# Kernel tuning notes

Measured on AMD Instinct MI355X. Metric: run time of the kernel, lower is better.

## Reference

```python
import jax, jax.numpy as jnp
import numpy as np
from jax import lax

KERNEL = 15
IGNORE = 255


def setup_inputs() -> dict:
    key = jax.random.key(0)
    k1, k2 = jax.random.split(key)
    B, C, H, W = 32, 2, 480, 864
    logits = jax.random.normal(k1, (B, C, H, W), dtype=jnp.float32)
    labels = jax.random.randint(k2, (B, H, W), 0, 2, dtype=jnp.int32)
    return {"logits": logits, "labels": labels}


def _boundary_edgemap(labels):
    # labels: [B, H, W] int32 with values in {0, 1, IGNORE}
    lbl = labels.astype(jnp.int32)
    # np_label = label*255, with ignore pixels set to 0 (matches cv2 path)
    np_label = jnp.where(lbl == IGNORE, 0, lbl * 255)
    win = (1, KERNEL, KERNEL)
    strides = (1, 1, 1)
    # cv2.erode with ones kernel == 15x15 min filter (border value +inf -> pad 255)
    erosion = lax.reduce_window(np_label, jnp.int32(255), lax.min, win, strides, "SAME")
    # cv2.dilate == 15x15 max filter (border value -inf -> pad 0)
    dilation = lax.reduce_window(np_label, jnp.int32(0), lax.max, win, strides, "SAME")
    boundary = dilation - erosion  # >0 exactly on the morphological boundary band
    edgemap = jnp.where(boundary > 0, lbl, IGNORE)
    edgemap = jnp.where(lbl == IGNORE, IGNORE, edgemap)
    return edgemap


def reference(logits, labels):
    # logits: [B, C, H, W] log-probabilities, labels: [B, H, W]
    edgemap = _boundary_edgemap(labels)  # [B, H, W]
    valid = edgemap != IGNORE
    tgt = jnp.where(valid, edgemap, 0)  # safe index for ignored pixels
    # gather logits[b, tgt, h, w] -> [B, H, W]
    picked = jnp.take_along_axis(logits, tgt[:, None, :, :], axis=1)[:, 0]
    # NLLLoss with ignore_index: mean of -logp over valid pixels
    n_valid = jnp.maximum(jnp.sum(valid), 1)
    loss = -jnp.sum(jnp.where(valid, picked, 0.0)) / n_valid.astype(logits.dtype)
    return loss
```

## Files before the change

### kernel.cpp

```cpp
#include <hip/hip_runtime.h>


namespace {
constexpr int B_ = 32;
constexpr int H_ = 480;
constexpr int W_ = 864;
constexpr int HW = H_ * W_;
constexpr int R_ = 7;
constexpr int OC = 50;
constexpr int TH_ = 32;
constexpr int LH = TH_ + 2 * R_;
constexpr int NSX = (W_ + OC - 1) / OC;
constexpr int NSY = H_ / TH_;
constexpr int NTILE = B_ * NSY * NSX;
constexpr int WPB = 4;
constexpr int NBLKP = NTILE / WPB;
}

__device__ __forceinline__ unsigned hwin15(unsigned x) {
  unsigned a = x | __shfl_down(x, 1, 64);
  a |= __shfl_down(a, 2, 64);
  a |= __shfl_down(a, 4, 64);
  a |= __shfl_down(a, 7, 64);
  return __shfl_up(a, 7, 64);
}

extern "C" __global__ __launch_bounds__(256, 6)
void boundary_loss_main(const float* __restrict__ logits,
                        const int* __restrict__ labels,
                        double2* __restrict__ partials)
{
  __shared__ double red_s[WPB];
  __shared__ unsigned red_c[WPB];

  const int tid = threadIdx.x;
  const int lane = tid & 63;
  const int wv = tid >> 6;
  const int t = blockIdx.x * WPB + wv;
  const int b  = t / (NSY * NSX);
  const int rr = t - b * (NSY * NSX);
  const int sy = rr / NSX;
  const int sx = rr - sy * NSX;

  const int gr0 = sy * TH_;
  const int col = sx * OC - R_ + lane;
  const bool colok = (col >= 0) && (col < W_);
  const int colc = col < 0 ? 0 : (col >= W_ ? W_ - 1 : col);

  const int* __restrict__ lab = labels + b * HW;
  const float* __restrict__ lg = logits + (size_t)(2 * b) * HW;

  unsigned f0 = 0, f1 = 0, f2 = 0, c0 = 0, c1 = 0, c2 = 0;
#pragma unroll
  for (int a = 0; a < LH; ++a) {
    const int gr = gr0 - R_ + a;
    const int grc = gr < 0 ? 0 : (gr >= H_ ? H_ - 1 : gr);
    const int v = lab[grc * W_ + colc];
    unsigned f = (unsigned)((v == 0) | (v == 255)) | ((unsigned)(v == 1) << 1);
    const unsigned c = (unsigned)(v == 1) | ((unsigned)(v == 255) << 1);
    if (gr < 0 || gr >= H_) f = 0;
    const int sh = 2 * (a & 15);
    if (a < 16)      { f0 |= f << sh; c0 |= c << sh; }
    else if (a < 32) { f1 |= f << sh; c1 |= c << sh; }
    else             { f2 |= f << sh; c2 |= c << sh; }
  }
  if (!colok) { f0 = f1 = f2 = 0; }

  const unsigned h0 = hwin15(f0);
  const unsigned h1 = hwin15(f1);
  const unsigned h2 = hwin15(f2);

  unsigned long long A  = (unsigned long long)h0 | ((unsigned long long)h1 << 32);
  unsigned long long Bv = (unsigned long long)h1 | ((unsigned long long)h2 << 32);
  A  |= A  >> 2;  A  |= A  >> 4;  A  |= A  >> 8;  A  |= A  >> 14;
  Bv |= Bv >> 2;  Bv |= Bv >> 4;  Bv |= Bv >> 8;  Bv |= Bv >> 14;

  double lsum = 0.0;
  unsigned lcnt = 0;
  const bool outlane = (lane >= R_) && (lane < R_ + OC) && colok;
  if (outlane) {
    int lgoff = gr0 * W_ + colc;
#pragma unroll
    for (int o = 0; o < TH_; ++o, lgoff += W_) {
      const unsigned fb = (o < 18) ? ((unsigned)(A >> (2 * o)) & 3u)
                                   : ((unsigned)(Bv >> (2 * (o - 16))) & 3u);
      const int ar = o + R_;
      const unsigned creg = (ar < 16) ? c0 : (ar < 32 ? c1 : c2);
      const unsigned cb = (creg >> (2 * (ar & 15))) & 3u;
      const bool ok = (fb == 3u) && ((cb & 2u) == 0u);
      const float val = lg[lgoff + (int)(cb & 1u) * HW];
      lsum += ok ? (double)val : 0.0;
      lcnt += ok ? 1u : 0u;
    }
  }

#pragma unroll
  for (int off = 32; off > 0; off >>= 1) {
    lsum += __shfl_down(lsum, off, 64);
    lcnt += __shfl_down(lcnt, off, 64);
  }
  if ((tid & 63) == 0) { red_s[wv] = lsum; red_c[wv] = lcnt; }
  __syncthreads();
  if (tid == 0) {
    const double s = red_s[0] + red_s[1] + red_s[2] + red_s[3];
    const double c = (double)(red_c[0] + red_c[1] + red_c[2] + red_c[3]);
    partials[blockIdx.x] = make_double2(s, c);
  }
}

extern "C" __global__ __launch_bounds__(1024)
void boundary_loss_final(const double2* __restrict__ partials,
                         float* __restrict__ out)
{
  __shared__ double red_s[16];
  __shared__ double red_c[16];
  const int tid = threadIdx.x;
  double s = 0.0, c = 0.0;
  for (int i = tid; i < NBLKP; i += 1024) {
    const double2 p = partials[i];
    s += p.x;
    c += p.y;
  }
#pragma unroll
  for (int off = 32; off > 0; off >>= 1) {
    s += __shfl_down(s, off, 64);
    c += __shfl_down(c, off, 64);
  }
  const int wave = tid >> 6;
  if ((tid & 63) == 0) { red_s[wave] = s; red_c[wave] = c; }
  __syncthreads();
  if (tid == 0) {
    double ts = 0.0, tc = 0.0;
#pragma unroll
    for (int i = 0; i < 16; ++i) { ts += red_s[i]; tc += red_c[i]; }
    if (tc < 1.0) tc = 1.0;
    out[0] = (float)(-ts / tc);
  }
}

extern "C" void kernel_launch(void* const* d_in, const int* in_sizes, int n_in,
                              void* d_out, int out_size, void* d_ws, size_t ws_size,
                              hipStream_t stream)
{
  const float* logits = (const float*)d_in[0];
  const int* labels = (const int*)d_in[1];
  float* out = (float*)d_out;
  double2* partials = (double2*)d_ws;

  boundary_loss_main<<<dim3(NBLKP), 256, 0, stream>>>(logits, labels, partials);
  boundary_loss_final<<<1, 1024, 0, stream>>>(partials, out);
}
```

Before: 196.2 us.

## Vectorize tiles to 4 columns per lane with int4/float4 loads

Each lane now handles four adjacent columns, loading labels as int4 and both logit channels as float4. Tiles become 8 rows by 216 columns, so the horizontal 15-wide dilation is built from two-lane shuffles on 64-bit packed masks and vertical halo overhead changes. Both logit channels are loaded unconditionally instead of gathering the selected one, which removes per-pixel scalar gathers at the cost of more register pressure, doubled logit traffic, and a larger relative vertical halo (8 rows with 14 halo rows).

Result: slower. 221.0 us (+12.6%).

```diff
diff --git a/kernel.cpp b/kernel.cpp
--- a/kernel.cpp
+++ b/kernel.cpp
@@ -7,25 +7,24 @@
 constexpr int W_ = 864;
 constexpr int HW = H_ * W_;
 constexpr int R_ = 7;
-constexpr int OC = 50;
-constexpr int TH_ = 32;
+constexpr int TH_ = 8;
 constexpr int LH = TH_ + 2 * R_;
-constexpr int NSX = (W_ + OC - 1) / OC;
+constexpr int SW = 216;
+constexpr int NSX = W_ / SW;
 constexpr int NSY = H_ / TH_;
+constexpr int WPB = 4;
 constexpr int NTILE = B_ * NSY * NSX;
-constexpr int WPB = 4;
 constexpr int NBLKP = NTILE / WPB;
 }
 
-__device__ __forceinline__ unsigned hwin15(unsigned x) {
-  unsigned a = x | __shfl_down(x, 1, 64);
-  a |= __shfl_down(a, 2, 64);
-  a |= __shfl_down(a, 4, 64);
-  a |= __shfl_down(a, 7, 64);
-  return __shfl_up(a, 7, 64);
+__device__ __forceinline__ unsigned long long shfl_up64(unsigned long long x, int d) {
+  return __shfl_up(x, d, 64);
+}
+__device__ __forceinline__ unsigned long long shfl_dn64(unsigned long long x, int d) {
+  return __shfl_down(x, d, 64);
 }
 
-extern "C" __global__ __launch_bounds__(256, 6)
+extern "C" __global__ __launch_bounds__(256, 4)
 void boundary_loss_main(const float* __restrict__ logits,
                         const int* __restrict__ labels,
                         double2* __restrict__ partials)
@@ -37,60 +36,104 @@
   const int lane = tid & 63;
   const int wv = tid >> 6;
   const int t = blockIdx.x * WPB + wv;
-  const int b  = t / (NSY * NSX);
+  const int b = t / (NSY * NSX);
   const int rr = t - b * (NSY * NSX);
-  const int sy = rr / NSX;
-  const int sx = rr - sy * NSX;
+  const int sy = rr >> 2;
+  const int sx = rr & 3;
 
   const int gr0 = sy * TH_;
-  const int col = sx * OC - R_ + lane;
-  const bool colok = (col >= 0) && (col < W_);
-  const int colc = col < 0 ? 0 : (col >= W_ ? W_ - 1 : col);
+  const int wb = sx * SW - 8;
+  const int cb0 = wb + 4 * lane;
+  const bool colinb = (cb0 >= 0) && (cb0 + 3 < W_);
+  const int cbc = colinb ? cb0 : (cb0 < 0 ? 0 : W_ - 4);
 
-  const int* __restrict__ lab = labels + b * HW;
+  const int* __restrict__ lab = labels + b * HW + cbc;
   const float* __restrict__ lg = logits + (size_t)(2 * b) * HW;
 
-  unsigned f0 = 0, f1 = 0, f2 = 0, c0 = 0, c1 = 0, c2 = 0;
+  int4 lv[LH];
 #pragma unroll
   for (int a = 0; a < LH; ++a) {
-    const int gr = gr0 - R_ + a;
-    const int grc = gr < 0 ? 0 : (gr >= H_ ? H_ - 1 : gr);
-    const int v = lab[grc * W_ + colc];
-    unsigned f = (unsigned)((v == 0) | (v == 255)) | ((unsigned)(v == 1) << 1);
-    const unsigned c = (unsigned)(v == 1) | ((unsigned)(v == 255) << 1);
-    if (gr < 0 || gr >= H_) f = 0;
-    const int sh = 2 * (a & 15);
-    if (a < 16)      { f0 |= f << sh; c0 |= c << sh; }
-    else if (a < 32) { f1 |= f << sh; c1 |= c << sh; }
-    else             { f2 |= f << sh; c2 |= c << sh; }
+    int gr = gr0 - R_ + a;
+    gr = gr < 0 ? 0 : (gr >= H_ ? H_ - 1 : gr);
+    lv[a] = *(const int4*)(lab + gr * W_);
   }
-  if (!colok) { f0 = f1 = f2 = 0; }
 
-  const unsigned h0 = hwin15(f0);
-  const unsigned h1 = hwin15(f1);
-  const unsigned h2 = hwin15(f2);
+  unsigned long long f0 = 0, f1 = 0, f2 = 0, f3 = 0;
+  unsigned cp0 = 0, cp1 = 0, cp2 = 0, cp3 = 0;
+#pragma unroll
+  for (int a = 0; a < LH; ++a) {
+    const int4 v = lv[a];
+    const unsigned e1x = (v.x == 1), e1y = (v.y == 1),
+                   e1z = (v.z == 1), e1w = (v.w == 1);
+    f0 |= (unsigned long long)(1u + e1x) << (2 * a);
+    f1 |= (unsigned long long)(1u + e1y) << (2 * a);
+    f2 |= (unsigned long long)(1u + e1z) << (2 * a);
+    f3 |= (unsigned long long)(1u + e1w) << (2 * a);
+    if (a >= R_ && a < R_ + TH_) {
+      const int sh = 2 * (a - R_);
+      cp0 |= (e1x | ((unsigned)(v.x == 255) << 1)) << sh;
+      cp1 |= (e1y | ((unsigned)(v.y == 255) << 1)) << sh;
+      cp2 |= (e1z | ((unsigned)(v.z == 255) << 1)) << sh;
+      cp3 |= (e1w | ((unsigned)(v.w == 255) << 1)) << sh;
+    }
+  }
+  {
+    const int tv = gr0 == 0 ? R_ : 0;
+    const int hi = LH < (487 - gr0) ? LH : (487 - gr0);
+    unsigned long long rm = ((1ull << (2 * (hi - tv))) - 1ull) << (2 * tv);
+    if (!colinb) rm = 0;
+    f0 &= rm; f1 &= rm; f2 &= rm; f3 &= rm;
+  }
 
-  unsigned long long A  = (unsigned long long)h0 | ((unsigned long long)h1 << 32);
-  unsigned long long Bv = (unsigned long long)h1 | ((unsigned long long)h2 << 32);
-  A  |= A  >> 2;  A  |= A  >> 4;  A  |= A  >> 8;  A  |= A  >> 14;
-  Bv |= Bv >> 2;  Bv |= Bv >> 4;  Bv |= Bv >> 8;  Bv |= Bv >> 14;
+  const bool outl = (lane >= 2) && (lane < 56);
+  float4 g0[TH_], g1[TH_];
+  if (outl) {
+    const float* pg = lg + (size_t)gr0 * W_ + cb0;
+#pragma unroll
+    for (int o = 0; o < TH_; ++o) {
+      g0[o] = *(const float4*)(pg + o * W_);
+      g1[o] = *(const float4*)(pg + o * W_ + HW);
+    }
+  }
+
+  const unsigned long long allf = f0 | f1 | f2 | f3;
+  const unsigned long long s2 = f2 | f3, s3 = f1 | s2;
+  const unsigned long long p2 = f0 | f1, p3 = p2 | f2;
+  const unsigned long long core =
+      shfl_up64(allf, 1) | allf | shfl_dn64(allf, 1);
+  unsigned long long w0 = core | shfl_up64(s3, 2);
+  unsigned long long w1 = core | shfl_up64(s2, 2) | shfl_dn64(f0, 2);
+  unsigned long long w2 = core | shfl_up64(f3, 2) | shfl_dn64(p2, 2);
+  unsigned long long w3 = core | shfl_dn64(p3, 2);
+
+  w0 |= w0 >> 2;  w0 |= w0 >> 4;  w0 |= w0 >> 8;  w0 |= w0 >> 14;
+  w1 |= w1 >> 2;  w1 |= w1 >> 4;  w1 |= w1 >> 8;  w1 |= w1 >> 14;
+  w2 |= w2 >> 2;  w2 |= w2 >> 4;  w2 |= w2 >> 8;  w2 |= w2 >> 14;
+  w3 |= w3 >> 2;  w3 |= w3 >> 4;  w3 |= w3 >> 8;  w3 |= w3 >> 14;
 
   double lsum = 0.0;
   unsigned lcnt = 0;
-  const bool outlane = (lane >= R_) && (lane < R_ + OC) && colok;
-  if (outlane) {
-    int lgoff = gr0 * W_ + colc;
+  if (outl) {
 #pragma unroll
-    for (int o = 0; o < TH_; ++o, lgoff += W_) {
-      const unsigned fb = (o < 18) ? ((unsigned)(A >> (2 * o)) & 3u)
-                                   : ((unsigned)(Bv >> (2 * (o - 16))) & 3u);
-      const int ar = o + R_;
-      const unsigned creg = (ar < 16) ? c0 : (ar < 32 ? c1 : c2);
-      const unsigned cb = (creg >> (2 * (ar & 15))) & 3u;
-      const bool ok = (fb == 3u) && ((cb & 2u) == 0u);
-      const float val = lg[lgoff + (int)(cb & 1u) * HW];
-      lsum += ok ? (double)val : 0.0;
-      lcnt += ok ? 1u : 0u;
+    for (int o = 0; o < TH_; ++o) {
+      const unsigned b0 = (unsigned)(w0 >> (2 * o)) & 3u;
+      const unsigned b1 = (unsigned)(w1 >> (2 * o)) & 3u;
+      const unsigned b2 = (unsigned)(w2 >> (2 * o)) & 3u;
+      const unsigned b3 = (unsigned)(w3 >> (2 * o)) & 3u;
+      const unsigned q0 = (cp0 >> (2 * o)) & 3u;
+      const unsigned q1 = (cp1 >> (2 * o)) & 3u;
+      const unsigned q2 = (cp2 >> (2 * o)) & 3u;
+      const unsigned q3 = (cp3 >> (2 * o)) & 3u;
+      const float4 a = g0[o], c = g1[o];
+      const bool k0 = (b0 == 3u) && !(q0 & 2u);
+      const bool k1 = (b1 == 3u) && !(q1 & 2u);
+      const bool k2 = (b2 == 3u) && !(q2 & 2u);
+      const bool k3 = (b3 == 3u) && !(q3 & 2u);
+      lsum += k0 ? (double)((q0 & 1u) ? c.x : a.x) : 0.0;
+      lsum += k1 ? (double)((q1 & 1u) ? c.y : a.y) : 0.0;
+      lsum += k2 ? (double)((q2 & 1u) ? c.z : a.z) : 0.0;
+      lsum += k3 ? (double)((q3 & 1u) ? c.w : a.w) : 0.0;
+      lcnt += (unsigned)k0 + k1 + k2 + k3;
     }
   }
 
```

## Restructure boundary loss into 216-wide block tiles with vectorized loads and LDS bitplanes

Applied to the files above, without the earlier changes.

Each block now handles a 32x216 tile. Waves cooperatively load label rows as int4, packing four columns per lane into 2-bit flags, and build the horizontal window with neighbour shuffles. Per-column bitmasks go through a shared-memory plane so each wave can run the vertical window over its 8 output rows. Logits for both classes are prefetched unconditionally as float4 before the label work, and block IDs are swizzled across XCDs. This cuts redundant halo loads and scalar gathers, at the cost of reading both logit channels and a sync plus more LDS and registers per block.

Measured after the change: 199.9 us. No clear change (+1.9%).

```diff
diff --git a/kernel.cpp b/kernel.cpp
--- a/kernel.cpp
+++ b/kernel.cpp
@@ -7,90 +7,144 @@
 constexpr int W_ = 864;
 constexpr int HW = H_ * W_;
 constexpr int R_ = 7;
-constexpr int OC = 50;
 constexpr int TH_ = 32;
 constexpr int LH = TH_ + 2 * R_;
-constexpr int NSX = (W_ + OC - 1) / OC;
+constexpr int SW = 216;
+constexpr int NSX = W_ / SW;
 constexpr int NSY = H_ / TH_;
-constexpr int NTILE = B_ * NSY * NSX;
-constexpr int WPB = 4;
-constexpr int NBLKP = NTILE / WPB;
-}
-
-__device__ __forceinline__ unsigned hwin15(unsigned x) {
-  unsigned a = x | __shfl_down(x, 1, 64);
-  a |= __shfl_down(a, 2, 64);
-  a |= __shfl_down(a, 4, 64);
-  a |= __shfl_down(a, 7, 64);
-  return __shfl_up(a, 7, 64);
-}
-
-extern "C" __global__ __launch_bounds__(256, 6)
+constexpr int NBLK = B_ * NSY * NSX;
+constexpr int ROWP = 50;
+}
+
+typedef unsigned long long u64;
+
+extern "C" __global__ __launch_bounds__(256, 4)
 void boundary_loss_main(const float* __restrict__ logits,
                         const int* __restrict__ labels,
                         double2* __restrict__ partials)
 {
-  __shared__ double red_s[WPB];
-  __shared__ unsigned red_c[WPB];
+  __shared__ unsigned short plane[64][ROWP];
+  __shared__ double red_s[4];
+  __shared__ unsigned red_c[4];
 
   const int tid = threadIdx.x;
   const int lane = tid & 63;
   const int wv = tid >> 6;
-  const int t = blockIdx.x * WPB + wv;
-  const int b  = t / (NSY * NSX);
-  const int rr = t - b * (NSY * NSX);
-  const int sy = rr / NSX;
-  const int sx = rr - sy * NSX;
-
+  const int bid = blockIdx.x;
+  const int lb = (bid & 7) * (NBLK / 8) + (bid >> 3);
+  const int b = lb / (NSY * NSX);
+  const int rr = lb - b * (NSY * NSX);
+  const int sy = rr >> 2;
+  const int sx = rr & 3;
   const int gr0 = sy * TH_;
-  const int col = sx * OC - R_ + lane;
-  const bool colok = (col >= 0) && (col < W_);
-  const int colc = col < 0 ? 0 : (col >= W_ ? W_ - 1 : col);
+  const int colbase = sx * SW;
 
   const int* __restrict__ lab = labels + b * HW;
   const float* __restrict__ lg = logits + (size_t)(2 * b) * HW;
 
-  unsigned f0 = 0, f1 = 0, f2 = 0, c0 = 0, c1 = 0, c2 = 0;
-#pragma unroll
-  for (int a = 0; a < LH; ++a) {
-    const int gr = gr0 - R_ + a;
-    const int grc = gr < 0 ? 0 : (gr >= H_ ? H_ - 1 : gr);
-    const int v = lab[grc * W_ + colc];
-    unsigned f = (unsigned)((v == 0) | (v == 255)) | ((unsigned)(v == 1) << 1);
-    const unsigned c = (unsigned)(v == 1) | ((unsigned)(v == 255) << 1);
-    if (gr < 0 || gr >= H_) f = 0;
-    const int sh = 2 * (a & 15);
-    if (a < 16)      { f0 |= f << sh; c0 |= c << sh; }
-    else if (a < 32) { f1 |= f << sh; c1 |= c << sh; }
-    else             { f2 |= f << sh; c2 |= c << sh; }
-  }
-  if (!colok) { f0 = f1 = f2 = 0; }
-
-  const unsigned h0 = hwin15(f0);
-  const unsigned h1 = hwin15(f1);
-  const unsigned h2 = hwin15(f2);
-
-  unsigned long long A  = (unsigned long long)h0 | ((unsigned long long)h1 << 32);
-  unsigned long long Bv = (unsigned long long)h1 | ((unsigned long long)h2 << 32);
-  A  |= A  >> 2;  A  |= A  >> 4;  A  |= A  >> 8;  A  |= A  >> 14;
-  Bv |= Bv >> 2;  Bv |= Bv >> 4;  Bv |= Bv >> 8;  Bv |= Bv >> 14;
+  const bool outl = (lane >= 2) && (lane < 56);
+  float4 ga[8], gc[8];
+  {
+    const float* pg = lg + (size_t)(gr0 + 8 * wv) * W_ + (colbase + 4 * (lane - 2));
+    if (outl) {
+#pragma unroll
+      for (int o = 0; o < 8; ++o) {
+        ga[o] = *(const float4*)(pg + (size_t)o * W_);
+        gc[o] = *(const float4*)(pg + (size_t)o * W_ + HW);
+      }
+    }
+  }
+
+  const int r_lo = 12 * wv;
+  const int nr = (wv == 3) ? 10 : 12;
+  const int cb0 = colbase - 8 + 4 * lane;
+  const bool labok = (lane < 58) && (cb0 >= 0) && (cb0 + 3 < W_);
+  const int* labp = lab + (labok ? cb0 : 0);
+
+  unsigned f0 = 0, f1 = 0, f2 = 0, f3 = 0;
+  unsigned c0 = 0, c1 = 0, c2 = 0, c3 = 0;
+#pragma unroll
+  for (int k = 0; k < 12; ++k) {
+    if (k < nr) {
+      const int a = r_lo + k;
+      const int gr = gr0 - R_ + a;
+      const bool rowok = (gr >= 0) && (gr < H_);
+      const int grc = rowok ? gr : (gr < 0 ? 0 : H_ - 1);
+      const int4 v = *(const int4*)(labp + grc * W_);
+      const unsigned m = (labok && rowok) ? 3u : 0u;
+      const int sh = 2 * k;
+      f0 |= (((v.x == 1) ? 2u : 1u) & m) << sh;
+      f1 |= (((v.y == 1) ? 2u : 1u) & m) << sh;
+      f2 |= (((v.z == 1) ? 2u : 1u) & m) << sh;
+      f3 |= (((v.w == 1) ? 2u : 1u) & m) << sh;
+      c0 |= (((v.x == 1) ? 1u : 0u) | ((v.x == 255) ? 2u : 0u)) << sh;
+      c1 |= (((v.y == 1) ? 1u : 0u) | ((v.y == 255) ? 2u : 0u)) << sh;
+      c2 |= (((v.z == 1) ? 1u : 0u) | ((v.z == 255) ? 2u : 0u)) << sh;
+      c3 |= (((v.w == 1) ? 1u : 0u) | ((v.w == 255) ? 2u : 0u)) << sh;
+    }
+  }
+
+  const unsigned allf = f0 | f1 | f2 | f3;
+  const unsigned s2 = f2 | f3, s3 = f1 | s2;
+  const unsigned p2 = f0 | f1, p3 = p2 | f2;
+  const unsigned core = __shfl_up(allf, 1, 64) | allf | __shfl_down(allf, 1, 64);
+  const unsigned w0 = core | __shfl_up(s3, 2, 64);
+  const unsigned w1 = core | __shfl_up(s2, 2, 64) | __shfl_down(f0, 2, 64);
+  const unsigned w2 = core | __shfl_up(f3, 2, 64) | __shfl_down(p2, 2, 64);
+  const unsigned w3 = core | __shfl_down(p3, 2, 64);
+
+#pragma unroll
+  for (int k = 0; k < 12; ++k) {
+    if (k < nr) {
+      const int sh = 2 * k;
+      const unsigned hb = ((w0 >> sh) & 3u) | (((w1 >> sh) & 3u) << 2) |
+                          (((w2 >> sh) & 3u) << 4) | (((w3 >> sh) & 3u) << 6);
+      const unsigned cby = ((c0 >> sh) & 3u) | (((c1 >> sh) & 3u) << 2) |
+                           (((c2 >> sh) & 3u) << 4) | (((c3 >> sh) & 3u) << 6);
+      plane[lane][r_lo + k] = (unsigned short)(hb | (cby << 8));
+    }
+  }
+  __syncthreads();
+
+  unsigned q[12];
+  {
+    const unsigned* pq = (const unsigned*)&plane[lane][8 * wv];
+#pragma unroll
+    for (int i = 0; i < 12; ++i) q[i] = pq[i];
+  }
+
+#define HP(i) ((u64)((q[i] & 0xFFu) | ((q[i] >> 8) & 0xFF00u)))
+#define CPAIR(i) ((u64)(((q[i] >> 8) & 0xFFu) | ((q[i] >> 24) << 8)))
+  u64 L = HP(0) | (HP(1) << 16) | (HP(2) << 32) | (HP(3) << 48);
+  u64 M = HP(4) | (HP(5) << 16) | (HP(6) << 32) | (HP(7) << 48);
+  u64 Hh = HP(8) | (HP(9) << 16) | (HP(10) << 32) | (HP(11) << 48);
+  L |= (L >> 8) | (M << 56);   M |= (M >> 8) | (Hh << 56);   Hh |= Hh >> 8;
+  L |= (L >> 16) | (M << 48);  M |= (M >> 16) | (Hh << 48);
+  L |= (L >> 32) | (M << 32);  M |= (M >> 32) | (Hh << 32);
+  const u64 F = L | (L >> 56) | (M << 8);
+  const u64 C = (u64)(q[3] >> 24)
+              | (CPAIR(4) << 8) | (CPAIR(5) << 24) | (CPAIR(6) << 40)
+              | ((u64)((q[7] >> 8) & 0xFFu) << 56);
+#undef HP
+#undef CPAIR
 
   double lsum = 0.0;
   unsigned lcnt = 0;
-  const bool outlane = (lane >= R_) && (lane < R_ + OC) && colok;
-  if (outlane) {
-    int lgoff = gr0 * W_ + colc;
-#pragma unroll
-    for (int o = 0; o < TH_; ++o, lgoff += W_) {
-      const unsigned fb = (o < 18) ? ((unsigned)(A >> (2 * o)) & 3u)
-                                   : ((unsigned)(Bv >> (2 * (o - 16))) & 3u);
-      const int ar = o + R_;
-      const unsigned creg = (ar < 16) ? c0 : (ar < 32 ? c1 : c2);
-      const unsigned cb = (creg >> (2 * (ar & 15))) & 3u;
-      const bool ok = (fb == 3u) && ((cb & 2u) == 0u);
-      const float val = lg[lgoff + (int)(cb & 1u) * HW];
-      lsum += ok ? (double)val : 0.0;
-      lcnt += ok ? 1u : 0u;
+  if (outl) {
+#pragma unroll
+    for (int o = 0; o < 8; ++o) {
+      const unsigned Fb = (unsigned)(F >> (8 * o)) & 0xFFu;
+      const unsigned Cb = (unsigned)(C >> (8 * o)) & 0xFFu;
+      const float4 A = ga[o], Cc = gc[o];
+      const bool k0 = ((Fb & 3u) == 3u) && !(Cb & 2u);
+      const bool k1 = (((Fb >> 2) & 3u) == 3u) && !((Cb >> 2) & 2u);
+      const bool k2 = (((Fb >> 4) & 3u) == 3u) && !((Cb >> 4) & 2u);
+      const bool k3 = (((Fb >> 6) & 3u) == 3u) && !((Cb >> 6) & 2u);
+      lsum += k0 ? (double)((Cb & 1u) ? Cc.x : A.x) : 0.0;
+      lsum += k1 ? (double)(((Cb >> 2) & 1u) ? Cc.y : A.y) : 0.0;
+      lsum += k2 ? (double)(((Cb >> 4) & 1u) ? Cc.z : A.z) : 0.0;
+      lsum += k3 ? (double)(((Cb >> 6) & 1u) ? Cc.w : A.w) : 0.0;
+      lcnt += (unsigned)k0 + k1 + k2 + k3;
     }
   }
 
@@ -104,7 +158,7 @@
   if (tid == 0) {
     const double s = red_s[0] + red_s[1] + red_s[2] + red_s[3];
     const double c = (double)(red_c[0] + red_c[1] + red_c[2] + red_c[3]);
-    partials[blockIdx.x] = make_double2(s, c);
+    partials[bid] = make_double2(s, c);
   }
 }
 
@@ -116,7 +170,7 @@
   __shared__ double red_c[16];
   const int tid = threadIdx.x;
   double s = 0.0, c = 0.0;
-  for (int i = tid; i < NBLKP; i += 1024) {
+  for (int i = tid; i < NBLK; i += 1024) {
     const double2 p = partials[i];
     s += p.x;
     c += p.y;
@@ -147,6 +201,6 @@
   float* out = (float*)d_out;
   double2* partials = (double2*)d_ws;
 
-  boundary_loss_main<<<dim3(NBLKP), 256, 0, stream>>>(logits, labels, partials);
+  boundary_loss_main<<<dim3(NBLK), 256, 0, stream>>>(logits, labels, partials);
   boundary_loss_final<<<1, 1024, 0, stream>>>(partials, out);
 }
```
